# Optimization experiments

Measured on AMD Instinct MI355X. Metric: run time of the kernel, lower is better.

Reference implementation:

```python
import jax, jax.numpy as jnp
import numpy as np

NEG_INF = -1e9


def setup_inputs() -> dict:
    key = jax.random.key(0)
    ks = jax.random.split(key, 7)
    N, Q, C = 16, 4096, 77
    D, Dc, H, S = 512, 768, 8, 64
    scale = 0.02
    return {
        "query": jax.random.normal(ks[0], (N, Q, D), jnp.float32),
        "context": jax.random.normal(ks[1], (N, C, Dc), jnp.float32),
        "Wq": jax.random.normal(ks[2], (D, H, S), jnp.float32) * scale,
        "Wk": jax.random.normal(ks[3], (Dc, H, S), jnp.float32) * scale,
        "Wv": jax.random.normal(ks[4], (Dc, H, S), jnp.float32) * scale,
        "Wo": jax.random.normal(ks[5], (H, S, D), jnp.float32) * scale,
        "bo": jnp.zeros((D,), jnp.float32),
    }


def reference(query, context, Wq, Wk, Wv, Wo, bo):
    # Projections: split hidden dim into heads.
    q = jnp.einsum('NQD,DHS->NQHS', query, Wq)      # [N,Q,H,S]
    k = jnp.einsum('NCD,DHS->NCHS', context, Wk)    # [N,C,H,S]
    v = jnp.einsum('NCD,DHS->NCHS', context, Wv)    # [N,C,H,S]
    size_per_head = q.shape[-1]
    # Attention scores [N,H,Q,C], scaled by 1/sqrt(S).
    scores = jnp.einsum('NQHS,NCHS->NHQC', q, k) * (size_per_head ** -0.5)
    weights = jax.nn.softmax(scores, axis=3)
    out = jnp.einsum('NHQC,NCHS->NQHS', weights, v)  # [N,Q,H,S]
    # Merge heads back to model dim with output bias.
    return jnp.einsum('NQHS,HSD->NQD', out, Wo) + bo
```

## Files before the change

kernel.cpp:

```cpp
#include <hip/hip_runtime.h>

typedef unsigned short u16;
typedef unsigned int u32;
typedef __bf16 bf16_t;
typedef bf16_t bf16x8 __attribute__((ext_vector_type(8)));
typedef float floatx4 __attribute__((ext_vector_type(4)));

__device__ __forceinline__ float bf2f(u16 h) {
    union { unsigned u; float f; } v;
    v.u = ((unsigned)h) << 16;
    return v.f;
}

__device__ __forceinline__ u16 f2bf(float f) {
    union { float f; unsigned u; } v;
    v.f = f;
    unsigned r = v.u + 0x7fffu + ((v.u >> 16) & 1u);
    return (u16)(r >> 16);
}

typedef __attribute__((address_space(1))) const u32 gu32;
typedef __attribute__((address_space(3))) u32 lu32;
__device__ __forceinline__ void gload16(const void* g, void* l) {
    __builtin_amdgcn_global_load_lds((gu32*)g, (lu32*)l, 16, 0, 0);
}

__global__ void transpose_one(const float* __restrict__ W, u16* __restrict__ Wt,
                              int K, int N) {
    int idx = blockIdx.x * 256 + threadIdx.x;
    if (idx >= K * N) return;
    int nrow = idx / K;
    int k = idx - nrow * K;
    Wt[idx] = f2bf(W[k * N + nrow]);
}

__global__ void transpose_kv(const float* __restrict__ Wk, const float* __restrict__ Wv,
                             u16* __restrict__ Wt) {
    int idx = blockIdx.x * 256 + threadIdx.x;
    if (idx >= 1024 * 768) return;
    int nrow = idx / 768;
    int k = idx - nrow * 768;
    Wt[idx] = f2bf((nrow < 512) ? Wk[k * 512 + nrow] : Wv[k * 512 + (nrow - 512)]);
}

__global__ void transpose_v(const u16* __restrict__ kv, u16* __restrict__ vt) {
    int idx = blockIdx.x * 256 + threadIdx.x;
    if (idx >= 16 * 8 * 64 * 96) return;
    int c  = idx % 96;
    int t1 = idx / 96;
    int s  = t1 & 63;
    int t2 = t1 >> 6;
    int h  = t2 & 7;
    int n  = t2 >> 3;
    u16 val = 0;
    if (c < 77) val = kv[((long)(n * 77 + c)) * 1024 + 512 + h * 64 + s];
    vt[idx] = val;
}

__global__ void convert_bf16(const float* __restrict__ src, u16* __restrict__ dst,
                             long n8) {
    long i = (long)blockIdx.x * blockDim.x + threadIdx.x;
    const long stride = (long)gridDim.x * blockDim.x;
    for (; i < n8; i += stride) {
        float4 f0 = *(const float4*)(src + i * 8);
        float4 f1 = *(const float4*)(src + i * 8 + 4);
        union { u16 h[8]; uint4 u; } pk;
        pk.h[0] = f2bf(f0.x); pk.h[1] = f2bf(f0.y);
        pk.h[2] = f2bf(f0.z); pk.h[3] = f2bf(f0.w);
        pk.h[4] = f2bf(f1.x); pk.h[5] = f2bf(f1.y);
        pk.h[6] = f2bf(f1.z); pk.h[7] = f2bf(f1.w);
        *(uint4*)(dst + i * 8) = pk.u;
    }
}

template <bool OUT_F32>
__global__ __launch_bounds__(512, 2) void gemm256(
    const u16* __restrict__ A, const u16* __restrict__ Bt,
    void* __restrict__ C_, const float* __restrict__ bias,
    int M, int K, int N, int ntl2)
{
    __shared__ u16 As[2][256 * 64];
    __shared__ u16 Bs[2][256 * 64];

    const int tid  = threadIdx.x;
    const int lane = tid & 63;
    const int wave = tid >> 6;
    const int quad = lane >> 4;
    const int l16  = lane & 15;
    const int wr   = wave & 1;
    const int wc   = wave >> 1;

    const int nwg = gridDim.x;
    const int wg  = blockIdx.x;
    const int t   = (wg & 7) * (nwg >> 3) + (wg >> 3);
    const long bm = (long)(t >> ntl2) * 256;
    const long bn = (long)(t & ((1 << ntl2) - 1)) * 256;

    floatx4 acc[8][4] = {};

    auto stage = [&](int b, int k0) {
        #pragma unroll
        for (int p = 0; p < 4; ++p) {
            int ch = p * 512 + tid;
            int r  = ch >> 3;
            int cs = (ch & 7) ^ (r & 7);
            gload16(A + (bm + r) * K + k0 + cs * 8,
                    &As[b][(p * 512 + wave * 64) * 8]);
        }
        #pragma unroll
        for (int p = 0; p < 4; ++p) {
            int ch = p * 512 + tid;
            int r  = ch >> 3;
            int cs = (ch & 7) ^ (r & 7);
            gload16(Bt + (bn + r) * K + k0 + cs * 8,
                    &Bs[b][(p * 512 + wave * 64) * 8]);
        }
    };

    const int nk = K >> 6;
    stage(0, 0);
    asm volatile("s_waitcnt vmcnt(0)" ::: "memory");
    __builtin_amdgcn_s_barrier();

    for (int tt = 0; tt < nk; ++tt) {
        const int cb = tt & 1;
        const u16* Ab = As[cb];
        const u16* Bb = Bs[cb];

        bf16x8 bfr[4][2];

        #pragma unroll
        for (int p = 0; p < 4; ++p) {
            bf16x8 af[2][2];
            #pragma unroll
            for (int ii = 0; ii < 2; ++ii) {
                int row = wr * 128 + (p * 2 + ii) * 16 + l16;
                #pragma unroll
                for (int kk = 0; kk < 2; ++kk)
                    af[ii][kk] = *(const bf16x8*)(
                        Ab + row * 64 + (((kk * 4) + quad) ^ (row & 7)) * 8);
            }
            if (p == 0) {
                #pragma unroll
                for (int j = 0; j < 4; ++j) {
                    int row = wc * 64 + j * 16 + l16;
                    #pragma unroll
                    for (int kk = 0; kk < 2; ++kk)
                        bfr[j][kk] = *(const bf16x8*)(
                            Bb + row * 64 + (((kk * 4) + quad) ^ (row & 7)) * 8);
                }
                if (tt + 1 < nk) stage(cb ^ 1, (tt + 1) << 6);
            }
            asm volatile("s_waitcnt lgkmcnt(0)" ::: "memory");
            __builtin_amdgcn_sched_barrier(0);
            __builtin_amdgcn_s_setprio(1);
            #pragma unroll
            for (int ii = 0; ii < 2; ++ii)
                #pragma unroll
                for (int j = 0; j < 4; ++j)
                    #pragma unroll
                    for (int kk = 0; kk < 2; ++kk)
                        acc[p * 2 + ii][j] = __builtin_amdgcn_mfma_f32_16x16x32_bf16(
                            af[ii][kk], bfr[j][kk], acc[p * 2 + ii][j], 0, 0, 0);
            __builtin_amdgcn_s_setprio(0);
            if (p == 3)
                asm volatile("s_waitcnt vmcnt(0)" ::: "memory");
            __builtin_amdgcn_s_barrier();
        }
    }

    float bj[4];
    #pragma unroll
    for (int j = 0; j < 4; ++j)
        bj[j] = bias ? bias[bn + wc * 64 + j * 16 + l16] : 0.f;

    #pragma unroll
    for (int i = 0; i < 8; ++i) {
        #pragma unroll
        for (int r = 0; r < 4; ++r) {
            long row = bm + wr * 128 + i * 16 + quad * 4 + r;
            #pragma unroll
            for (int j = 0; j < 4; ++j) {
                long col = bn + wc * 64 + j * 16 + l16;
                float val = acc[i][j][r] + bj[j];
                if (OUT_F32) ((float*)C_)[row * N + col] = val;
                else         ((u16*)C_)[row * N + col] = f2bf(val);
            }
        }
    }
}

#define TM 128
#define TN 256
#define TK 32

template <bool A_F32, bool OUT_F32>
__global__ __launch_bounds__(512, 4) void gemm_bt(
    const void* __restrict__ A_, const u16* __restrict__ Bt,
    void* __restrict__ C_, const float* __restrict__ bias,
    int M, int K, int N, int ntl2)
{
    constexpr int AB = A_F32 ? TM * TK * 4 : TM * TK * 2;
    constexpr int BB = TN * TK * 2;
    __shared__ __align__(16) char smem[2 * (AB + BB)];

    const int tid  = threadIdx.x;
    const int lane = tid & 63;
    const int wave = tid >> 6;
    const int quad = lane >> 4;
    const int l16  = lane & 15;
    const int wm   = (wave & 1) * 64;
    const int wn   = (wave >> 1) * 64;

    const int nwg = gridDim.x;
    const int wg  = blockIdx.x;
    const int t   = (wg & 7) * (nwg >> 3) + (wg >> 3);
    const long bm = (long)(t >> ntl2) * TM;
    const long bn = (long)(t & ((1 << ntl2) - 1)) * TN;

    const float* Af = (const float*)A_;
    const u16*   Ab = (const u16*)A_;
    const long   Mm1 = (long)M - 1;

    floatx4 acc[4][4] = {};

    auto stage = [&](int b, int k0) {
        char* Abase = smem + b * (AB + BB);
        u16*  Bb    = (u16*)(Abase + AB);
        #pragma unroll
        for (int p = 0; p < 2; ++p) {
            int ch  = p * 512 + tid;
            int row = ch >> 2;
            int pc  = (ch & 3) ^ ((row >> 1) & 3);
            gload16(Bt + (bn + row) * K + k0 + pc * 8,
                    Bb + (p * 512 + wave * 64) * 8);
        }
        if (A_F32) {
            #pragma unroll
            for (int p = 0; p < 2; ++p) {
                int ch  = p * 512 + tid;
                int row = ch >> 3;
                int pcs = (ch & 7) ^ (row & 7);
                long gr = bm + row; if (gr > Mm1) gr = Mm1;
                gload16(Af + gr * K + k0 + pcs * 4,
                        (float*)Abase + (p * 512 + wave * 64) * 4);
            }
        } else {
            int row = tid >> 2;
            int pc  = (tid & 3) ^ ((row >> 1) & 3);
            long gr = bm + row; if (gr > Mm1) gr = Mm1;
            gload16(Ab + gr * K + k0 + pc * 8,
                    (u16*)Abase + (wave * 64) * 8);
        }
    };

    const int nk = K / TK;
    stage(0, 0);

    for (int tt = 0; tt < nk; ++tt) {
        const int cb = tt & 1;
        if (tt + 1 < nk) {
            stage(cb ^ 1, (tt + 1) * TK);
            if (A_F32) asm volatile("s_waitcnt vmcnt(4)" ::: "memory");
            else       asm volatile("s_waitcnt vmcnt(3)" ::: "memory");
        } else {
            asm volatile("s_waitcnt vmcnt(0)" ::: "memory");
        }
        __builtin_amdgcn_s_barrier();
        __builtin_amdgcn_sched_barrier(0);

        const char* Abase = smem + cb * (AB + BB);
        const u16*  Bb    = (const u16*)(Abase + AB);

        bf16x8 af[4], bfr[4];
        #pragma unroll
        for (int i = 0; i < 4; ++i) {
            int row = wm + i * 16 + l16;
            if (A_F32) {
                const char* arow = Abase + (size_t)row * 128;
                int x = row & 7;
                float4 f0 = *(const float4*)(arow + (((quad * 2)     ^ x) * 16));
                float4 f1 = *(const float4*)(arow + (((quad * 2 + 1) ^ x) * 16));
                union { bf16_t h[8]; bf16x8 v; } pk;
                pk.h[0] = (bf16_t)f0.x; pk.h[1] = (bf16_t)f0.y;
                pk.h[2] = (bf16_t)f0.z; pk.h[3] = (bf16_t)f0.w;
                pk.h[4] = (bf16_t)f1.x; pk.h[5] = (bf16_t)f1.y;
                pk.h[6] = (bf16_t)f1.z; pk.h[7] = (bf16_t)f1.w;
                af[i] = pk.v;
            } else {
                int pcs = quad ^ ((row >> 1) & 3);
                af[i] = *(const bf16x8*)((const u16*)Abase + row * 32 + pcs * 8);
            }
        }
        #pragma unroll
        for (int j = 0; j < 4; ++j) {
            int row = wn + j * 16 + l16;
            int pcs = quad ^ ((row >> 1) & 3);
            bfr[j] = *(const bf16x8*)(Bb + row * 32 + pcs * 8);
        }
        #pragma unroll
        for (int i = 0; i < 4; ++i)
            #pragma unroll
            for (int j = 0; j < 4; ++j)
                acc[i][j] = __builtin_amdgcn_mfma_f32_16x16x32_bf16(
                    af[i], bfr[j], acc[i][j], 0, 0, 0);

        __builtin_amdgcn_s_barrier();
    }

    #pragma unroll
    for (int i = 0; i < 4; ++i) {
        #pragma unroll
        for (int r = 0; r < 4; ++r) {
            long row = bm + wm + i * 16 + quad * 4 + r;
            if (row >= M) continue;
            #pragma unroll
            for (int j = 0; j < 4; ++j) {
                long col = bn + wn + j * 16 + l16;
                float val = acc[i][j][r];
                if (bias) val += bias[col];
                if (OUT_F32) ((float*)C_)[row * N + col] = val;
                else         ((u16*)C_)[row * N + col] = f2bf(val);
            }
        }
    }
}

__global__ __launch_bounds__(256) void attn_kernel(
    const u16* __restrict__ qb,
    const u16* __restrict__ kvb,
    const u16* __restrict__ vt,
    u16* __restrict__ ob)
{
    const int QL = 4096, HS = 512;
    const int q0 = blockIdx.x * 256;
    const int h  = blockIdx.y;
    const int n  = blockIdx.z;

    __shared__ u16 sQP[128 * 104];
    __shared__ u16 ks [80 * 72];
    __shared__ u16 vts[64 * 104];

    const int tid  = threadIdx.x;
    const int lane = tid & 63;
    const int wave = tid >> 6;
    const int quad = lane >> 4;
    const int l16  = lane & 15;
    const int wm   = wave * 32;

    const u16* kbase = kvb + (long)n * 77 * 1024 + h * 64;
    for (int v = tid; v < 640; v += 256) {
        int c = v >> 3, g = (v & 7) * 8;
        uint4 val = make_uint4(0, 0, 0, 0);
        if (c < 77) val = *(const uint4*)(kbase + (long)c * 1024 + g);
        *(uint4*)(&ks[c * 72 + g]) = val;
    }
    const u16* vtbase = vt + (long)((n * 8 + h) * 64) * 96;
    for (int v = tid; v < 768; v += 256) {
        int r = v / 12, c8 = v - r * 12;
        *(uint4*)(&vts[r * 104 + c8 * 8]) = *(const uint4*)(vtbase + v * 8);
    }
    __syncthreads();

    const bool v4ok = (l16 < 13);

    for (int it = 0; it < 2; ++it) {
        const long qrow0 = (long)q0 + it * 128;
        const u16* qbase = qb + ((long)n * QL + qrow0) * HS + h * 64;
        u16*       obase = ob + ((long)n * QL + qrow0) * HS + h * 64;

        #pragma unroll
        for (int p = 0; p < 4; ++p) {
            int v = tid + p * 256;
            int r = v >> 3, g = (v & 7) * 8;
            *(uint4*)(&sQP[r * 72 + g]) = *(const uint4*)(qbase + (long)r * HS + g);
        }
        __syncthreads();

        floatx4 accS[2][5] = {};
        #pragma unroll
        for (int kk = 0; kk < 2; ++kk) {
            bf16x8 aq[2], bk[5];
            #pragma unroll
            for (int t = 0; t < 2; ++t)
                aq[t] = *(const bf16x8*)(&sQP[(wm + t * 16 + l16) * 72 + kk * 32 + quad * 8]);
            #pragma unroll
            for (int j = 0; j < 5; ++j)
                bk[j] = *(const bf16x8*)(&ks[(j * 16 + l16) * 72 + kk * 32 + quad * 8]);
            #pragma unroll
            for (int t = 0; t < 2; ++t)
                #pragma unroll
                for (int j = 0; j < 5; ++j)
                    accS[t][j] = __builtin_amdgcn_mfma_f32_16x16x32_bf16(
                        aq[t], bk[j], accS[t][j], 0, 0, 0);
        }

        float pw[2][5][4];
        #pragma unroll
        for (int t = 0; t < 2; ++t) {
            #pragma unroll
            for (int r = 0; r < 4; ++r) {
                float v0 = accS[t][0][r] * 0.125f;
                float v1 = accS[t][1][r] * 0.125f;
                float v2 = accS[t][2][r] * 0.125f;
                float v3 = accS[t][3][r] * 0.125f;
                float v4 = v4ok ? accS[t][4][r] * 0.125f : -1e30f;
                float mx = fmaxf(fmaxf(fmaxf(v0, v1), fmaxf(v2, v3)), v4);
                mx = fmaxf(mx, __shfl_xor(mx, 1));
                mx = fmaxf(mx, __shfl_xor(mx, 2));
                mx = fmaxf(mx, __shfl_xor(mx, 4));
                mx = fmaxf(mx, __shfl_xor(mx, 8));
                float e0 = __expf(v0 - mx), e1 = __expf(v1 - mx);
                float e2 = __expf(v2 - mx), e3 = __expf(v3 - mx);
                float e4 = __expf(v4 - mx);
                float sum = e0 + e1 + e2 + e3 + e4;
                sum += __shfl_xor(sum, 1);
                sum += __shfl_xor(sum, 2);
                sum += __shfl_xor(sum, 4);
                sum += __shfl_xor(sum, 8);
                float inv = 1.f / sum;
                pw[t][0][r] = e0 * inv; pw[t][1][r] = e1 * inv;
                pw[t][2][r] = e2 * inv; pw[t][3][r] = e3 * inv;
                pw[t][4][r] = e4 * inv;
            }
        }
        __syncthreads();

        #pragma unroll
        for (int t = 0; t < 2; ++t) {
            #pragma unroll
            for (int r = 0; r < 4; ++r) {
                int row = wm + t * 16 + quad * 4 + r;
                #pragma unroll
                for (int j = 0; j < 5; ++j)
                    sQP[row * 104 + j * 16 + l16] = f2bf(pw[t][j][r]);
                sQP[row * 104 + 80 + l16] = 0;
            }
        }
        __syncthreads();

        floatx4 accO[2][4] = {};
        #pragma unroll
        for (int kk = 0; kk < 3; ++kk) {
            bf16x8 aw[2], bv[4];
            #pragma unroll
            for (int t = 0; t < 2; ++t)
                aw[t] = *(const bf16x8*)(&sQP[(wm + t * 16 + l16) * 104 + kk * 32 + quad * 8]);
            #pragma unroll
            for (int j = 0; j < 4; ++j)
                bv[j] = *(const bf16x8*)(&vts[(j * 16 + l16) * 104 + kk * 32 + quad * 8]);
            #pragma unroll
            for (int t = 0; t < 2; ++t)
                #pragma unroll
                for (int j = 0; j < 4; ++j)
                    accO[t][j] = __builtin_amdgcn_mfma_f32_16x16x32_bf16(
                        aw[t], bv[j], accO[t][j], 0, 0, 0);
        }

        #pragma unroll
        for (int t = 0; t < 2; ++t)
            #pragma unroll
            for (int j = 0; j < 4; ++j)
                #pragma unroll
                for (int r = 0; r < 4; ++r) {
                    int row = wm + t * 16 + quad * 4 + r;
                    obase[(long)row * HS + j * 16 + l16] = f2bf(accO[t][j][r]);
                }
        __syncthreads();
    }
}

extern "C" void kernel_launch(void* const* d_in, const int* in_sizes, int n_in,
                              void* d_out, int out_size, void* d_ws, size_t ws_size,
                              hipStream_t stream) {
    const float* query   = (const float*)d_in[0];
    const float* context = (const float*)d_in[1];
    const float* Wq      = (const float*)d_in[2];
    const float* Wk      = (const float*)d_in[3];
    const float* Wv      = (const float*)d_in[4];
    const float* Wo      = (const float*)d_in[5];
    const float* bo      = (const float*)d_in[6];
    float* out = (float*)d_out;

    u16* q_ws  = (u16*)d_ws;
    u16* kv_ws = q_ws + 33554432;
    u16* WqT   = kv_ws + 1261568;
    u16* WkvT  = WqT + 262144;
    u16* WoT   = WkvT + 786432;
    u16* vt_ws = WkvT;

    u16* q_bf  = (u16*)d_out;

    transpose_one<<<(512 * 512 + 255) / 256, 256, 0, stream>>>(Wq, WqT, 512, 512);
    transpose_kv<<<(1024 * 768 + 255) / 256, 256, 0, stream>>>(Wk, Wv, WkvT);
    transpose_one<<<(512 * 512 + 255) / 256, 256, 0, stream>>>(Wo, WoT, 512, 512);

    convert_bf16<<<dim3(2048), 256, 0, stream>>>(query, q_bf, 4194304L);

    gemm256<false><<<dim3(512), 512, 0, stream>>>(
        q_bf, WqT, (void*)q_ws, nullptr, 65536, 512, 512, 1);
    gemm_bt<true, false><<<dim3(40), 512, 0, stream>>>(
        (const void*)context, WkvT, (void*)kv_ws, nullptr, 1232, 768, 1024, 2);
    transpose_v<<<(16 * 8 * 64 * 96 + 255) / 256, 256, 0, stream>>>(kv_ws, vt_ws);
    attn_kernel<<<dim3(16, 8, 16), 256, 0, stream>>>(q_ws, kv_ws, vt_ws, q_ws);
    gemm256<true><<<dim3(512), 512, 0, stream>>>(
        q_ws, WoT, (void*)out, bo, 65536, 512, 512, 1);
}
```

Baseline: 436.5 us.

## Fuse query conversion into Q GEMM and restructure attention per-wave

Drops the separate fp32-to-bf16 pass over the query and feeds the fp32 query directly into the gemm_bt kernel (fp32 A path) for the Q projection. The 1/sqrt(S) softmax scale is folded into the transposed Wq weights. The attention kernel now uses 512 threads with each wave loading its own Q rows into registers and keeping a private LDS buffer for P, so most block barriers go away; output rows are staged through LDS for coalesced 16-byte stores. In exchange the Q GEMM uses a smaller tile kernel instead of the 256x256 one, and attention needs more LDS per block.

Measured after the change: 408.5 us. 1.07x faster.

```diff
diff --git a/kernel.cpp b/kernel.cpp
--- a/kernel.cpp
+++ b/kernel.cpp
@@ -26,12 +26,12 @@
 }
 
 __global__ void transpose_one(const float* __restrict__ W, u16* __restrict__ Wt,
-                              int K, int N) {
+                              int K, int N, float scale) {
     int idx = blockIdx.x * 256 + threadIdx.x;
     if (idx >= K * N) return;
     int nrow = idx / K;
     int k = idx - nrow * K;
-    Wt[idx] = f2bf(W[k * N + nrow]);
+    Wt[idx] = f2bf(W[k * N + nrow] * scale);
 }
 
 __global__ void transpose_kv(const float* __restrict__ Wk, const float* __restrict__ Wv,
@@ -55,139 +55,6 @@
     u16 val = 0;
     if (c < 77) val = kv[((long)(n * 77 + c)) * 1024 + 512 + h * 64 + s];
     vt[idx] = val;
-}
-
-__global__ void convert_bf16(const float* __restrict__ src, u16* __restrict__ dst,
-                             long n8) {
-    long i = (long)blockIdx.x * blockDim.x + threadIdx.x;
-    const long stride = (long)gridDim.x * blockDim.x;
-    for (; i < n8; i += stride) {
-        float4 f0 = *(const float4*)(src + i * 8);
-        float4 f1 = *(const float4*)(src + i * 8 + 4);
-        union { u16 h[8]; uint4 u; } pk;
-        pk.h[0] = f2bf(f0.x); pk.h[1] = f2bf(f0.y);
-        pk.h[2] = f2bf(f0.z); pk.h[3] = f2bf(f0.w);
-        pk.h[4] = f2bf(f1.x); pk.h[5] = f2bf(f1.y);
-        pk.h[6] = f2bf(f1.z); pk.h[7] = f2bf(f1.w);
-        *(uint4*)(dst + i * 8) = pk.u;
-    }
-}
-
-template <bool OUT_F32>
-__global__ __launch_bounds__(512, 2) void gemm256(
-    const u16* __restrict__ A, const u16* __restrict__ Bt,
-    void* __restrict__ C_, const float* __restrict__ bias,
-    int M, int K, int N, int ntl2)
-{
-    __shared__ u16 As[2][256 * 64];
-    __shared__ u16 Bs[2][256 * 64];
-
-    const int tid  = threadIdx.x;
-    const int lane = tid & 63;
-    const int wave = tid >> 6;
-    const int quad = lane >> 4;
-    const int l16  = lane & 15;
-    const int wr   = wave & 1;
-    const int wc   = wave >> 1;
-
-    const int nwg = gridDim.x;
-    const int wg  = blockIdx.x;
-    const int t   = (wg & 7) * (nwg >> 3) + (wg >> 3);
-    const long bm = (long)(t >> ntl2) * 256;
-    const long bn = (long)(t & ((1 << ntl2) - 1)) * 256;
-
-    floatx4 acc[8][4] = {};
-
-    auto stage = [&](int b, int k0) {
-        #pragma unroll
-        for (int p = 0; p < 4; ++p) {
-            int ch = p * 512 + tid;
-            int r  = ch >> 3;
-            int cs = (ch & 7) ^ (r & 7);
-            gload16(A + (bm + r) * K + k0 + cs * 8,
-                    &As[b][(p * 512 + wave * 64) * 8]);
-        }
-        #pragma unroll
-        for (int p = 0; p < 4; ++p) {
-            int ch = p * 512 + tid;
-            int r  = ch >> 3;
-            int cs = (ch & 7) ^ (r & 7);
-            gload16(Bt + (bn + r) * K + k0 + cs * 8,
-                    &Bs[b][(p * 512 + wave * 64) * 8]);
-        }
-    };
-
-    const int nk = K >> 6;
-    stage(0, 0);
-    asm volatile("s_waitcnt vmcnt(0)" ::: "memory");
-    __builtin_amdgcn_s_barrier();
-
-    for (int tt = 0; tt < nk; ++tt) {
-        const int cb = tt & 1;
-        const u16* Ab = As[cb];
-        const u16* Bb = Bs[cb];
-
-        bf16x8 bfr[4][2];
-
-        #pragma unroll
-        for (int p = 0; p < 4; ++p) {
-            bf16x8 af[2][2];
-            #pragma unroll
-            for (int ii = 0; ii < 2; ++ii) {
-                int row = wr * 128 + (p * 2 + ii) * 16 + l16;
-                #pragma unroll
-                for (int kk = 0; kk < 2; ++kk)
-                    af[ii][kk] = *(const bf16x8*)(
-                        Ab + row * 64 + (((kk * 4) + quad) ^ (row & 7)) * 8);
-            }
-            if (p == 0) {
-                #pragma unroll
-                for (int j = 0; j < 4; ++j) {
-                    int row = wc * 64 + j * 16 + l16;
-                    #pragma unroll
-                    for (int kk = 0; kk < 2; ++kk)
-                        bfr[j][kk] = *(const bf16x8*)(
-                            Bb + row * 64 + (((kk * 4) + quad) ^ (row & 7)) * 8);
-                }
-                if (tt + 1 < nk) stage(cb ^ 1, (tt + 1) << 6);
-            }
-            asm volatile("s_waitcnt lgkmcnt(0)" ::: "memory");
-            __builtin_amdgcn_sched_barrier(0);
-            __builtin_amdgcn_s_setprio(1);
-            #pragma unroll
-            for (int ii = 0; ii < 2; ++ii)
-                #pragma unroll
-                for (int j = 0; j < 4; ++j)
-                    #pragma unroll
-                    for (int kk = 0; kk < 2; ++kk)
-                        acc[p * 2 + ii][j] = __builtin_amdgcn_mfma_f32_16x16x32_bf16(
-                            af[ii][kk], bfr[j][kk], acc[p * 2 + ii][j], 0, 0, 0);
-            __builtin_amdgcn_s_setprio(0);
-            if (p == 3)
-                asm volatile("s_waitcnt vmcnt(0)" ::: "memory");
-            __builtin_amdgcn_s_barrier();
-        }
-    }
-
-    float bj[4];
-    #pragma unroll
-    for (int j = 0; j < 4; ++j)
-        bj[j] = bias ? bias[bn + wc * 64 + j * 16 + l16] : 0.f;
-
-    #pragma unroll
-    for (int i = 0; i < 8; ++i) {
-        #pragma unroll
-        for (int r = 0; r < 4; ++r) {
-            long row = bm + wr * 128 + i * 16 + quad * 4 + r;
-            #pragma unroll
-            for (int j = 0; j < 4; ++j) {
-                long col = bn + wc * 64 + j * 16 + l16;
-                float val = acc[i][j][r] + bj[j];
-                if (OUT_F32) ((float*)C_)[row * N + col] = val;
-                else         ((u16*)C_)[row * N + col] = f2bf(val);
-            }
-        }
-    }
 }
 
 #define TM 128
@@ -326,7 +193,124 @@
     }
 }
 
-__global__ __launch_bounds__(256) void attn_kernel(
+template <bool OUT_F32>
+__global__ __launch_bounds__(512, 2) void gemm256(
+    const u16* __restrict__ A, const u16* __restrict__ Bt,
+    void* __restrict__ C_, const float* __restrict__ bias,
+    int M, int K, int N, int ntl2)
+{
+    __shared__ u16 As[2][256 * 64];
+    __shared__ u16 Bs[2][256 * 64];
+
+    const int tid  = threadIdx.x;
+    const int lane = tid & 63;
+    const int wave = tid >> 6;
+    const int quad = lane >> 4;
+    const int l16  = lane & 15;
+    const int wr   = wave & 1;
+    const int wc   = wave >> 1;
+
+    const int nwg = gridDim.x;
+    const int wg  = blockIdx.x;
+    const int t   = (wg & 7) * (nwg >> 3) + (wg >> 3);
+    const long bm = (long)(t >> ntl2) * 256;
+    const long bn = (long)(t & ((1 << ntl2) - 1)) * 256;
+
+    floatx4 acc[8][4] = {};
+
+    auto stage = [&](int b, int k0) {
+        #pragma unroll
+        for (int p = 0; p < 4; ++p) {
+            int ch = p * 512 + tid;
+            int r  = ch >> 3;
+            int cs = (ch & 7) ^ (r & 7);
+            gload16(A + (bm + r) * K + k0 + cs * 8,
+                    &As[b][(p * 512 + wave * 64) * 8]);
+        }
+        #pragma unroll
+        for (int p = 0; p < 4; ++p) {
+            int ch = p * 512 + tid;
+            int r  = ch >> 3;
+            int cs = (ch & 7) ^ (r & 7);
+            gload16(Bt + (bn + r) * K + k0 + cs * 8,
+                    &Bs[b][(p * 512 + wave * 64) * 8]);
+        }
+    };
+
+    const int nk = K >> 6;
+    stage(0, 0);
+    asm volatile("s_waitcnt vmcnt(0)" ::: "memory");
+    __builtin_amdgcn_s_barrier();
+
+    for (int tt = 0; tt < nk; ++tt) {
+        const int cb = tt & 1;
+        const u16* Ab = As[cb];
+        const u16* Bb = Bs[cb];
+
+        bf16x8 bfr[4][2];
+
+        #pragma unroll
+        for (int p = 0; p < 4; ++p) {
+            bf16x8 af[2][2];
+            #pragma unroll
+            for (int ii = 0; ii < 2; ++ii) {
+                int row = wr * 128 + (p * 2 + ii) * 16 + l16;
+                #pragma unroll
+                for (int kk = 0; kk < 2; ++kk)
+                    af[ii][kk] = *(const bf16x8*)(
+                        Ab + row * 64 + (((kk * 4) + quad) ^ (row & 7)) * 8);
+            }
+            if (p == 0) {
+                #pragma unroll
+                for (int j = 0; j < 4; ++j) {
+                    int row = wc * 64 + j * 16 + l16;
+                    #pragma unroll
+                    for (int kk = 0; kk < 2; ++kk)
+                        bfr[j][kk] = *(const bf16x8*)(
+                            Bb + row * 64 + (((kk * 4) + quad) ^ (row & 7)) * 8);
+                }
+                if (tt + 1 < nk) stage(cb ^ 1, (tt + 1) << 6);
+            }
+            asm volatile("s_waitcnt lgkmcnt(0)" ::: "memory");
+            __builtin_amdgcn_sched_barrier(0);
+            __builtin_amdgcn_s_setprio(1);
+            #pragma unroll
+            for (int ii = 0; ii < 2; ++ii)
+                #pragma unroll
+                for (int j = 0; j < 4; ++j)
+                    #pragma unroll
+                    for (int kk = 0; kk < 2; ++kk)
+                        acc[p * 2 + ii][j] = __builtin_amdgcn_mfma_f32_16x16x32_bf16(
+                            af[ii][kk], bfr[j][kk], acc[p * 2 + ii][j], 0, 0, 0);
+            __builtin_amdgcn_s_setprio(0);
+            if (p == 3)
+                asm volatile("s_waitcnt vmcnt(0)" ::: "memory");
+            __builtin_amdgcn_s_barrier();
+        }
+    }
+
+    float bj[4];
+    #pragma unroll
+    for (int j = 0; j < 4; ++j)
+        bj[j] = bias ? bias[bn + wc * 64 + j * 16 + l16] : 0.f;
+
+    #pragma unroll
+    for (int i = 0; i < 8; ++i) {
+        #pragma unroll
+        for (int r = 0; r < 4; ++r) {
+            long row = bm + wr * 128 + i * 16 + quad * 4 + r;
+            #pragma unroll
+            for (int j = 0; j < 4; ++j) {
+                long col = bn + wc * 64 + j * 16 + l16;
+                float val = acc[i][j][r] + bj[j];
+                if (OUT_F32) ((float*)C_)[row * N + col] = val;
+                else         ((u16*)C_)[row * N + col] = f2bf(val);
+            }
+        }
+    }
+}
+
+__global__ __launch_bounds__(512, 4) void attn_kernel(
     const u16* __restrict__ qb,
     const u16* __restrict__ kvb,
     const u16* __restrict__ vt,
@@ -337,136 +321,129 @@
     const int h  = blockIdx.y;
     const int n  = blockIdx.z;
 
-    __shared__ u16 sQP[128 * 104];
     __shared__ u16 ks [80 * 72];
     __shared__ u16 vts[64 * 104];
+    __shared__ u16 pS [8][32 * 104];
 
     const int tid  = threadIdx.x;
     const int lane = tid & 63;
     const int wave = tid >> 6;
     const int quad = lane >> 4;
     const int l16  = lane & 15;
-    const int wm   = wave * 32;
+
+    const long qrow = (long)n * QL + q0 + wave * 32;
+    bf16x8 aq[2][2];
+    #pragma unroll
+    for (int t = 0; t < 2; ++t)
+        #pragma unroll
+        for (int kk = 0; kk < 2; ++kk)
+            aq[t][kk] = *(const bf16x8*)(
+                qb + (qrow + t * 16 + l16) * HS + h * 64 + kk * 32 + quad * 8);
 
     const u16* kbase = kvb + (long)n * 77 * 1024 + h * 64;
-    for (int v = tid; v < 640; v += 256) {
+    for (int v = tid; v < 640; v += 512) {
         int c = v >> 3, g = (v & 7) * 8;
         uint4 val = make_uint4(0, 0, 0, 0);
         if (c < 77) val = *(const uint4*)(kbase + (long)c * 1024 + g);
         *(uint4*)(&ks[c * 72 + g]) = val;
     }
     const u16* vtbase = vt + (long)((n * 8 + h) * 64) * 96;
-    for (int v = tid; v < 768; v += 256) {
+    for (int v = tid; v < 768; v += 512) {
         int r = v / 12, c8 = v - r * 12;
         *(uint4*)(&vts[r * 104 + c8 * 8]) = *(const uint4*)(vtbase + v * 8);
     }
     __syncthreads();
 
+    floatx4 accS[2][5] = {};
+    #pragma unroll
+    for (int kk = 0; kk < 2; ++kk) {
+        bf16x8 bk[5];
+        #pragma unroll
+        for (int j = 0; j < 5; ++j)
+            bk[j] = *(const bf16x8*)(&ks[(j * 16 + l16) * 72 + kk * 32 + quad * 8]);
+        __builtin_amdgcn_s_setprio(1);
+        #pragma unroll
+        for (int t = 0; t < 2; ++t)
+            #pragma unroll
+            for (int j = 0; j < 5; ++j)
+                accS[t][j] = __builtin_amdgcn_mfma_f32_16x16x32_bf16(
+                    aq[t][kk], bk[j], accS[t][j], 0, 0, 0);
+        __builtin_amdgcn_s_setprio(0);
+    }
+
     const bool v4ok = (l16 < 13);
-
-    for (int it = 0; it < 2; ++it) {
-        const long qrow0 = (long)q0 + it * 128;
-        const u16* qbase = qb + ((long)n * QL + qrow0) * HS + h * 64;
-        u16*       obase = ob + ((long)n * QL + qrow0) * HS + h * 64;
-
-        #pragma unroll
-        for (int p = 0; p < 4; ++p) {
-            int v = tid + p * 256;
-            int r = v >> 3, g = (v & 7) * 8;
-            *(uint4*)(&sQP[r * 72 + g]) = *(const uint4*)(qbase + (long)r * HS + g);
-        }
-        __syncthreads();
-
-        floatx4 accS[2][5] = {};
-        #pragma unroll
-        for (int kk = 0; kk < 2; ++kk) {
-            bf16x8 aq[2], bk[5];
-            #pragma unroll
-            for (int t = 0; t < 2; ++t)
-                aq[t] = *(const bf16x8*)(&sQP[(wm + t * 16 + l16) * 72 + kk * 32 + quad * 8]);
-            #pragma unroll
-            for (int j = 0; j < 5; ++j)
-                bk[j] = *(const bf16x8*)(&ks[(j * 16 + l16) * 72 + kk * 32 + quad * 8]);
-            #pragma unroll
-            for (int t = 0; t < 2; ++t)
-                #pragma unroll
-                for (int j = 0; j < 5; ++j)
-                    accS[t][j] = __builtin_amdgcn_mfma_f32_16x16x32_bf16(
-                        aq[t], bk[j], accS[t][j], 0, 0, 0);
-        }
-
-        float pw[2][5][4];
-        #pragma unroll
-        for (int t = 0; t < 2; ++t) {
+    u16* pw = pS[wave];
+    #pragma unroll
+    for (int t = 0; t < 2; ++t) {
+        #pragma unroll
+        for (int r = 0; r < 4; ++r) {
+            float v0 = accS[t][0][r];
+            float v1 = accS[t][1][r];
+            float v2 = accS[t][2][r];
+            float v3 = accS[t][3][r];
+            float v4 = v4ok ? accS[t][4][r] : -1e30f;
+            float mx = fmaxf(fmaxf(fmaxf(v0, v1), fmaxf(v2, v3)), v4);
+            mx = fmaxf(mx, __shfl_xor(mx, 1));
+            mx = fmaxf(mx, __shfl_xor(mx, 2));
+            mx = fmaxf(mx, __shfl_xor(mx, 4));
+            mx = fmaxf(mx, __shfl_xor(mx, 8));
+            float e0 = __expf(v0 - mx), e1 = __expf(v1 - mx);
+            float e2 = __expf(v2 - mx), e3 = __expf(v3 - mx);
+            float e4 = __expf(v4 - mx);
+            float sum = e0 + e1 + e2 + e3 + e4;
+            sum += __shfl_xor(sum, 1);
+            sum += __shfl_xor(sum, 2);
+            sum += __shfl_xor(sum, 4);
+            sum += __shfl_xor(sum, 8);
+            float inv = 1.f / sum;
+            int row = t * 16 + quad * 4 + r;
+            pw[row * 104 +  0 + l16] = f2bf(e0 * inv);
+            pw[row * 104 + 16 + l16] = f2bf(e1 * inv);
+            pw[row * 104 + 32 + l16] = f2bf(e2 * inv);
+            pw[row * 104 + 48 + l16] = f2bf(e3 * inv);
+            pw[row * 104 + 64 + l16] = f2bf(e4 * inv);
+            pw[row * 104 + 80 + l16] = 0;
+        }
+    }
+
+    floatx4 accO[2][4] = {};
+    #pragma unroll
+    for (int kk = 0; kk < 3; ++kk) {
+        bf16x8 aw[2], bv[4];
+        #pragma unroll
+        for (int t = 0; t < 2; ++t)
+            aw[t] = *(const bf16x8*)(&pw[(t * 16 + l16) * 104 + kk * 32 + quad * 8]);
+        #pragma unroll
+        for (int j = 0; j < 4; ++j)
+            bv[j] = *(const bf16x8*)(&vts[(j * 16 + l16) * 104 + kk * 32 + quad * 8]);
+        __builtin_amdgcn_s_setprio(1);
+        #pragma unroll
+        for (int t = 0; t < 2; ++t)
+            #pragma unroll
+            for (int j = 0; j < 4; ++j)
+                accO[t][j] = __builtin_amdgcn_mfma_f32_16x16x32_bf16(
+                    aw[t], bv[j], accO[t][j], 0, 0, 0);
+        __builtin_amdgcn_s_setprio(0);
+    }
+
+    #pragma unroll
+    for (int t = 0; t < 2; ++t)
+        #pragma unroll
+        for (int j = 0; j < 4; ++j)
             #pragma unroll
             for (int r = 0; r < 4; ++r) {
-                float v0 = accS[t][0][r] * 0.125f;
-                float v1 = accS[t][1][r] * 0.125f;
-                float v2 = accS[t][2][r] * 0.125f;
-                float v3 = accS[t][3][r] * 0.125f;
-                float v4 = v4ok ? accS[t][4][r] * 0.125f : -1e30f;
-                float mx = fmaxf(fmaxf(fmaxf(v0, v1), fmaxf(v2, v3)), v4);
-                mx = fmaxf(mx, __shfl_xor(mx, 1));
-                mx = fmaxf(mx, __shfl_xor(mx, 2));
-                mx = fmaxf(mx, __shfl_xor(mx, 4));
-                mx = fmaxf(mx, __shfl_xor(mx, 8));
-                float e0 = __expf(v0 - mx), e1 = __expf(v1 - mx);
-                float e2 = __expf(v2 - mx), e3 = __expf(v3 - mx);
-                float e4 = __expf(v4 - mx);
-                float sum = e0 + e1 + e2 + e3 + e4;
-                sum += __shfl_xor(sum, 1);
-                sum += __shfl_xor(sum, 2);
-                sum += __shfl_xor(sum, 4);
-                sum += __shfl_xor(sum, 8);
-                float inv = 1.f / sum;
-                pw[t][0][r] = e0 * inv; pw[t][1][r] = e1 * inv;
-                pw[t][2][r] = e2 * inv; pw[t][3][r] = e3 * inv;
-                pw[t][4][r] = e4 * inv;
-            }
-        }
-        __syncthreads();
-
-        #pragma unroll
-        for (int t = 0; t < 2; ++t) {
-            #pragma unroll
-            for (int r = 0; r < 4; ++r) {
-                int row = wm + t * 16 + quad * 4 + r;
-                #pragma unroll
-                for (int j = 0; j < 5; ++j)
-                    sQP[row * 104 + j * 16 + l16] = f2bf(pw[t][j][r]);
-                sQP[row * 104 + 80 + l16] = 0;
-            }
-        }
-        __syncthreads();
-
-        floatx4 accO[2][4] = {};
-        #pragma unroll
-        for (int kk = 0; kk < 3; ++kk) {
-            bf16x8 aw[2], bv[4];
-            #pragma unroll
-            for (int t = 0; t < 2; ++t)
-                aw[t] = *(const bf16x8*)(&sQP[(wm + t * 16 + l16) * 104 + kk * 32 + quad * 8]);
-            #pragma unroll
-            for (int j = 0; j < 4; ++j)
-                bv[j] = *(const bf16x8*)(&vts[(j * 16 + l16) * 104 + kk * 32 + quad * 8]);
-            #pragma unroll
-            for (int t = 0; t < 2; ++t)
-                #pragma unroll
-                for (int j = 0; j < 4; ++j)
-                    accO[t][j] = __builtin_amdgcn_mfma_f32_16x16x32_bf16(
-                        aw[t], bv[j], accO[t][j], 0, 0, 0);
-        }
-
-        #pragma unroll
-        for (int t = 0; t < 2; ++t)
-            #pragma unroll
-            for (int j = 0; j < 4; ++j)
-                #pragma unroll
-                for (int r = 0; r < 4; ++r) {
-                    int row = wm + t * 16 + quad * 4 + r;
-                    obase[(long)row * HS + j * 16 + l16] = f2bf(accO[t][j][r]);
-                }
-        __syncthreads();
+                int row = t * 16 + quad * 4 + r;
+                pw[row * 72 + j * 16 + l16] = f2bf(accO[t][j][r]);
+            }
+
+    u16* obase = ob + qrow * HS + h * 64;
+    #pragma unroll
+    for (int k = 0; k < 4; ++k) {
+        int v   = k * 64 + lane;
+        int row = v >> 3;
+        int c8  = v & 7;
+        *(uint4*)(obase + (long)row * HS + c8 * 8) =
+            *(const uint4*)(&pw[row * 72 + c8 * 8]);
     }
 }
 
@@ -489,20 +466,16 @@
     u16* WoT   = WkvT + 786432;
     u16* vt_ws = WkvT;
 
-    u16* q_bf  = (u16*)d_out;
-
-    transpose_one<<<(512 * 512 + 255) / 256, 256, 0, stream>>>(Wq, WqT, 512, 512);
+    transpose_one<<<(512 * 512 + 255) / 256, 256, 0, stream>>>(Wq, WqT, 512, 512, 0.125f);
     transpose_kv<<<(1024 * 768 + 255) / 256, 256, 0, stream>>>(Wk, Wv, WkvT);
-    transpose_one<<<(512 * 512 + 255) / 256, 256, 0, stream>>>(Wo, WoT, 512, 512);
-
-    convert_bf16<<<dim3(2048), 256, 0, stream>>>(query, q_bf, 4194304L);
-
-    gemm256<false><<<dim3(512), 512, 0, stream>>>(
-        q_bf, WqT, (void*)q_ws, nullptr, 65536, 512, 512, 1);
+    transpose_one<<<(512 * 512 + 255) / 256, 256, 0, stream>>>(Wo, WoT, 512, 512, 1.0f);
+
+    gemm_bt<true, false><<<dim3(1024), 512, 0, stream>>>(
+        (const void*)query, WqT, (void*)q_ws, nullptr, 65536, 512, 512, 1);
     gemm_bt<true, false><<<dim3(40), 512, 0, stream>>>(
         (const void*)context, WkvT, (void*)kv_ws, nullptr, 1232, 768, 1024, 2);
     transpose_v<<<(16 * 8 * 64 * 96 + 255) / 256, 256, 0, stream>>>(kv_ws, vt_ws);
-    attn_kernel<<<dim3(16, 8, 16), 256, 0, stream>>>(q_ws, kv_ws, vt_ws, q_ws);
+    attn_kernel<<<dim3(16, 8, 16), 512, 0, stream>>>(q_ws, kv_ws, vt_ws, q_ws);
     gemm256<true><<<dim3(512), 512, 0, stream>>>(
         q_ws, WoT, (void*)out, bo, 65536, 512, 512, 1);
 }
```
